# Optimization experiments

Measured on AMD Instinct MI355X. Metric: run time of the kernel, lower is better.

## Reference

```python
import jax, jax.numpy as jnp
import numpy as np

B, C, T, Q = 4, 64, 128, 128   # batch, channels (emb_dim), frames, freq bins
K = 8                          # unfold kernel size (stride 1)
H = 128                        # SRU hidden size per direction
D_IN = C * K                   # SRU input size after unfold
L = Q - K + 1                  # unfolded sequence length
EPS = 1e-5


def setup_inputs() -> dict:
    key = jax.random.key(0)
    ks = jax.random.split(key, 6)
    s = 0.02
    return {
        "features": jax.random.normal(ks[0], (B, C, T, Q), jnp.float32),
        "ln_gamma": jnp.ones((C,), jnp.float32),
        "ln_beta": jnp.zeros((C,), jnp.float32),
        # SRU per-direction weights: W maps D_IN -> [x_tilde | f_gate | r_gate | highway], each H wide
        "w_fwd": jax.random.normal(ks[1], (D_IN, 4 * H), jnp.float32) * s,
        "b_fwd": jnp.zeros((2 * H,), jnp.float32),   # [b_f | b_r]
        "w_bwd": jax.random.normal(ks[2], (D_IN, 4 * H), jnp.float32) * s,
        "b_bwd": jnp.zeros((2 * H,), jnp.float32),
        # ConvTranspose1d weight in PyTorch layout [in_ch=2H, out_ch=C, K]
        "ct_w": jax.random.normal(ks[3], (2 * H, C, K), jnp.float32) * s,
        "ct_b": jnp.zeros((C,), jnp.float32),
    }


def _sru_dir(seq, W, b, reverse):
    """One SRU direction. seq: [N, L, D_IN] -> h: [N, L, H].
    c_t = f_t*c_{t-1} + (1-f_t)*x~_t ;  h_t = r_t*tanh(c_t) + (1-r_t)*x'_t
    (x' is the highway projection since input dim != hidden dim)."""
    U = seq @ W                                   # [N, L, 4H] -- dominant GEMM
    xt, f_pre, r_pre, xp = jnp.split(U, 4, axis=-1)
    bf, br = jnp.split(b, 2)
    f = jax.nn.sigmoid(f_pre + bf)
    r = jax.nn.sigmoid(r_pre + br)
    u = (1.0 - f) * xt
    if reverse:
        f = jnp.flip(f, 1)
        u = jnp.flip(u, 1)
    def combine(x, y):  # linear recurrence c = a*c_prev + b, y is the later element
        return (x[0] * y[0], x[1] * y[0] + y[1])
    c = jax.lax.associative_scan(combine, (f, u), axis=1)[1]
    if reverse:
        c = jnp.flip(c, 1)
    return r * jnp.tanh(c) + (1.0 - r) * xp


def reference(features, ln_gamma, ln_beta, w_fwd, b_fwd, w_bwd, b_bwd, ct_w, ct_b):
    # LayerNorm([C,1,1]): normalize over channel dim per (b,t,q)
    mu = jnp.mean(features, axis=1, keepdims=True)
    var = jnp.var(features, axis=1, keepdims=True)
    x = (features - mu) * jax.lax.rsqrt(var + EPS)
    x = x * ln_gamma[None, :, None, None] + ln_beta[None, :, None, None]

    N = B * T
    x = x.transpose(0, 2, 1, 3).reshape(N, C, Q)          # [B*T, C, Q]
    # nn.Unfold((K,1), stride 1): channel-major patch layout -> [N, C*K, L]
    u = jnp.stack([x[:, :, i:i + L] for i in range(K)], axis=2).reshape(N, C * K, L)
    seq = u.transpose(0, 2, 1)                            # [N, L, C*K]

    h = jnp.concatenate(
        [_sru_dir(seq, w_fwd, b_fwd, False), _sru_dir(seq, w_bwd, b_bwd, True)],
        axis=-1,
    )                                                      # [N, L, 2H]

    # ConvTranspose1d(2H -> C, K, stride=1) == full correlation with flipped kernel
    rhs = jnp.flip(ct_w, -1).transpose(1, 0, 2)           # [C, 2H, K]
    y = jax.lax.conv_general_dilated(
        h.transpose(0, 2, 1), rhs, (1,), [(K - 1, K - 1)],
        dimension_numbers=("NCH", "OIH", "NCH"),
    ) + ct_b[None, :, None]                               # [N, C, Q]

    y = y.reshape(B, T, C, Q).transpose(0, 2, 1, 3)       # [B, C, T, Q]
    return y + features
```

## Files before the change

kernel.cpp:

```cpp
#include <hip/hip_runtime.h>
#include <math.h>

#define BB 4
#define CC 64
#define TT 128
#define QQ 128
#define KK 8
#define HH 128
#define NN 512
#define LL 121
#define LPAD 135

typedef unsigned short ushort;
typedef __attribute__((ext_vector_type(8))) short short8;
typedef __attribute__((ext_vector_type(4))) float f32x4;
typedef __attribute__((ext_vector_type(4))) float float4v;

#define GLP(p) ((const __attribute__((address_space(1))) void*)(p))
#define LDP(p) ((__attribute__((address_space(3))) void*)(p))

__device__ __forceinline__ ushort f2bf(float x) {
  unsigned u = __float_as_uint(x);
  unsigned r = (u + 0x7FFFu + ((u >> 16) & 1u)) >> 16;
  return (ushort)r;
}

__global__ __launch_bounds__(256)
void prep_all(const float* __restrict__ f, const float* __restrict__ gamma,
              const float* __restrict__ beta, const float* __restrict__ wf,
              const float* __restrict__ wb, const float* __restrict__ ctw,
              ushort* __restrict__ xT, ushort* __restrict__ Wt,
              ushort* __restrict__ Bct, ushort* __restrict__ zpage) {
  int bid = blockIdx.x, tid = threadIdx.x;
  if (bid < 256) {
    int p = bid * 256 + tid;
    int q = p & (QQ - 1);
    int t = (p >> 7) & (TT - 1);
    int b = p >> 14;
    const float* base = f + (size_t)b * CC * TT * QQ + (size_t)t * QQ + q;
    float v[64];
#pragma unroll
    for (int c = 0; c < 64; ++c) v[c] = base[(size_t)c * TT * QQ];
    float s = 0.f, s2 = 0.f;
#pragma unroll
    for (int c = 0; c < 64; ++c) { s += v[c]; s2 += v[c] * v[c]; }
    float mu = s * (1.f / CC);
    float var = s2 * (1.f / CC) - mu * mu;
    float rs = rsqrtf(var + 1e-5f);
    int n = b * TT + t;
    ushort* dst = xT + (size_t)n * (CC * QQ) + (size_t)q * CC;
#pragma unroll
    for (int v8 = 0; v8 < 8; ++v8) {
      short8 ov;
#pragma unroll
      for (int e = 0; e < 8; ++e) {
        int c = v8 * 8 + e;
        ov[e] = (short)f2bf((v[c] - mu) * rs * gamma[c] + beta[c]);
      }
      *(short8*)(dst + v8 * 8) = ov;
    }
  } else if (bid < 2816) {
    int idx = (bid - 256) * 256 + tid;
    if (idx < 524288) {
      int r = idx >> 9, d = idx & 511;
      int k = d >> 6, c = d & 63;
      int dir = r >> 9, t = r & 511;
      int h = (t >> 7) * 32 + ((t >> 6) & 1) * 16 + (t & 15);
      int quad = (t >> 4) & 3;
      const float* w = dir ? wb : wf;
      Wt[idx] = f2bf(w[(size_t)(c * 8 + k) * 512 + quad * 128 + h]);
    } else {
      int i2 = idx - 524288;
      int c = i2 >> 11, d = i2 & 2047;
      int k = d >> 8, j = d & 255;
      Bct[i2] = f2bf(ctw[(size_t)j * (CC * KK) + c * KK + k]);
    }
  } else {
    if (tid < 128) ((unsigned*)zpage)[tid] = 0u;
  }
}

__global__ __launch_bounds__(256, 2)
void gemm_mfma(const ushort* __restrict__ xT, const ushort* __restrict__ Wt,
               const float* __restrict__ b_fwd, const float* __restrict__ b_bwd,
               ushort* __restrict__ hp, int n0) {
  __shared__ __align__(16) char smem[49152];
  ushort* As = (ushort*)smem;
  ushort* Bs = (ushort*)(smem + 16384);

  int tid = threadIdx.x;
  int nl = blockIdx.y;
  int r0 = blockIdx.x * 256;
  int lane = tid & 63, w = tid >> 6;
  int lrow = lane & 15, lk = lane >> 4;
  f32x4 acc[8][4] = {};
  const ushort* xTn = xT + (size_t)(n0 + nl) * (CC * QQ);
  for (int ks = 0; ks < 8; ++ks) {
    if (ks) __syncthreads();
#pragma unroll
    for (int i = 0; i < 4; ++i) {
      int p = i * 256 + tid;
      int row = p >> 3, s = (p & 7) ^ (row & 7);
      int grow = ((row & 0x0C) << 3) | ((row & 0x70) >> 2) | (row & 3);
      const ushort* g = xTn + (size_t)(grow + ks) * CC + s * 8;
      ushort* l = &As[(size_t)(i * 256 + (tid & 192)) * 8];
      __builtin_amdgcn_global_load_lds(GLP(g), LDP(l), 16, 0, 0);
    }
#pragma unroll
    for (int i = 0; i < 8; ++i) {
      int p = i * 256 + tid;
      int row = p >> 3, s = (p & 7) ^ (row & 7);
      const ushort* g = Wt + (size_t)(r0 + row) * 512 + ks * 64 + s * 8;
      ushort* l = &Bs[(size_t)(i * 256 + (tid & 192)) * 8];
      __builtin_amdgcn_global_load_lds(GLP(g), LDP(l), 16, 0, 0);
    }
    __syncthreads();
#pragma unroll
    for (int s = 0; s < 2; ++s) {
      short8 a[8], b[4];
#pragma unroll
      for (int m = 0; m < 8; ++m) {
        int r = m * 16 + lrow;
        int slot = (s * 4 + lk) ^ (r & 7);
        a[m] = *(const short8*)&As[r * 64 + slot * 8];
      }
#pragma unroll
      for (int nn = 0; nn < 4; ++nn) {
        int j = w * 64 + nn * 16 + lrow;
        int slot = (s * 4 + lk) ^ (j & 7);
        b[nn] = *(const short8*)&Bs[j * 64 + slot * 8];
      }
#pragma unroll
      for (int m = 0; m < 8; ++m)
#pragma unroll
        for (int nn = 0; nn < 4; ++nn)
          acc[m][nn] = __builtin_amdgcn_mfma_f32_16x16x32_bf16(
              a[m], b[nn], acc[m][nn], 0, 0, 0);
    }
  }
  int dirf = r0 >> 9;
  int hgroup = ((r0 & 511) >> 7) + (w >> 1);
  int h = hgroup * 32 + (w & 1) * 16 + lrow;
  const float* bias = dirf ? b_bwd : b_fwd;
  float bf = bias[h], br = bias[128 + h];

  float F = 1.f, U = 0.f;
  if (dirf == 0) {
#pragma unroll
    for (int m = 0; m < 8; ++m)
#pragma unroll
      for (int g = 0; g < 4; ++g) {
        int l = lk * 32 + m * 4 + g;
        float xt = acc[m][0][g], fp = acc[m][1][g];
        float fg = 1.f / (1.f + __expf(-(fp + bf)));
        float u = (1.f - fg) * xt;
        if (l > 120) { fg = 1.f; u = 0.f; }
        U = fg * U + u;
        F = fg * F;
        acc[m][0][g] = F; acc[m][1][g] = U;
      }
  } else {
#pragma unroll
    for (int m = 7; m >= 0; --m)
#pragma unroll
      for (int g = 3; g >= 0; --g) {
        int l = lk * 32 + m * 4 + g;
        float xt = acc[m][0][g], fp = acc[m][1][g];
        float fg = 1.f / (1.f + __expf(-(fp + bf)));
        float u = (1.f - fg) * xt;
        if (l > 120) { fg = 1.f; u = 0.f; }
        U = fg * U + u;
        F = fg * F;
        acc[m][0][g] = F; acc[m][1][g] = U;
      }
  }
  int e = dirf ? 3 - lk : lk;
  float lpU = 0.f;
#pragma unroll
  for (int j = 0; j < 4; ++j) {
    int jl = dirf ? 3 - j : j;
    float tF = __shfl(F, (jl << 4) + lrow);
    float tU = __shfl(U, (jl << 4) + lrow);
    if (j < e) lpU = tF * lpU + tU;
  }
  float cinit = lpU;
  ushort* hpn = hp + (size_t)nl * LPAD * 256;
  int colbase = dirf * 128 + hgroup * 32 + (w & 1) * 16;
#pragma unroll
  for (int m = 0; m < 8; ++m) {
#pragma unroll
    for (int g = 0; g < 4; ++g) {
      int l = lk * 32 + m * 4 + g;
      float c = acc[m][1][g] + acc[m][0][g] * cinit;
      float rp = acc[m][2][g];
      float rg = 1.f / (1.f + __expf(-(rp + br)));
      float e2 = __expf(2.f * c);
      float th = (e2 - 1.f) / (e2 + 1.f);
      float ho = rg * th + (1.f - rg) * acc[m][3][g];
      hpn[(size_t)(l + 7) * 256 + colbase + lrow] = f2bf(ho);
    }
  }
}

__global__ __launch_bounds__(256)
void conv_mfma(const ushort* __restrict__ hp, const ushort* __restrict__ Bct,
               const ushort* __restrict__ zpage, const float* __restrict__ ctb,
               const float* __restrict__ feat, float* __restrict__ out, int n0) {
  __shared__ ushort As[2][128 * 64];
  __shared__ ushort Bs[2][64 * 64];
  int tid = threadIdx.x;
  int nl = blockIdx.x;
  int lane = tid & 63, w = tid >> 6;
  int wr0 = (w >> 1) * 64, wc0 = (w & 1) * 32;
  int lrow = lane & 15, lk = lane >> 4;
  f32x4 acc[4][2] = {};
  const ushort* hpn = hp + (size_t)nl * LPAD * 256;

#define CONV_STAGE(KS, BSEL)                                               \
  {                                                                        \
    int kk_ = (KS) >> 2, j0_ = ((KS) & 3) * 64;                            \
    _Pragma("unroll")                                                      \
    for (int i = 0; i < 4; ++i) {                                          \
      int p = i * 256 + tid;                                               \
      int row = p >> 3, s = (p & 7) ^ (row & 7);                           \
      int rr = row - kk_;                                                  \
      const ushort* g = ((unsigned)rr <= 120u)                             \
          ? hpn + (size_t)(rr + 7) * 256 + j0_ + s * 8                     \
          : zpage + s * 8;                                                 \
      ushort* l = &As[BSEL][(size_t)(i * 256 + (tid & 192)) * 8];          \
      __builtin_amdgcn_global_load_lds(GLP(g), LDP(l), 16, 0, 0);          \
    }                                                                      \
    _Pragma("unroll")                                                      \
    for (int i = 0; i < 2; ++i) {                                          \
      int p = i * 256 + tid;                                               \
      int row = p >> 3, s = (p & 7) ^ (row & 7);                           \
      const ushort* g = Bct + (size_t)row * 2048 + (KS) * 64 + s * 8;      \
      ushort* l = &Bs[BSEL][(size_t)(i * 256 + (tid & 192)) * 8];          \
      __builtin_amdgcn_global_load_lds(GLP(g), LDP(l), 16, 0, 0);          \
    }                                                                      \
  }

  CONV_STAGE(0, 0);
  __syncthreads();
  for (int ks = 0; ks < 32; ++ks) {
    int cur = ks & 1;
    if (ks < 31) CONV_STAGE(ks + 1, cur ^ 1);
#pragma unroll
    for (int s = 0; s < 2; ++s) {
      short8 a[4], b[2];
#pragma unroll
      for (int m = 0; m < 4; ++m) {
        int r = wr0 + m * 16 + lrow;
        int slot = (s * 4 + lk) ^ (r & 7);
        a[m] = *(const short8*)&As[cur][r * 64 + slot * 8];
      }
#pragma unroll
      for (int nn = 0; nn < 2; ++nn) {
        int c = wc0 + nn * 16 + lrow;
        int slot = (s * 4 + lk) ^ (c & 7);
        b[nn] = *(const short8*)&Bs[cur][c * 64 + slot * 8];
      }
#pragma unroll
      for (int m = 0; m < 4; ++m)
#pragma unroll
        for (int nn = 0; nn < 2; ++nn)
          acc[m][nn] = __builtin_amdgcn_mfma_f32_16x16x32_bf16(
              a[m], b[nn], acc[m][nn], 0, 0, 0);
    }
    __syncthreads();
  }
#undef CONV_STAGE
  int n = n0 + nl;
  int b = n >> 7, t = n & 127;
#pragma unroll
  for (int m = 0; m < 4; ++m) {
    int q0 = wr0 + m * 16 + lk * 4;
#pragma unroll
    for (int nn = 0; nn < 2; ++nn) {
      int c = wc0 + nn * 16 + lrow;
      size_t idx = (size_t)b * (CC * TT * QQ) + (size_t)c * (TT * QQ)
                 + (size_t)t * QQ + q0;
      float4v fv = *(const float4v*)&feat[idx];
      float cb = ctb[c];
      float4v ov;
#pragma unroll
      for (int g = 0; g < 4; ++g) ov[g] = acc[m][nn][g] + cb + fv[g];
      *(float4v*)&out[idx] = ov;
    }
  }
}

extern "C" void kernel_launch(void* const* d_in, const int* in_sizes, int n_in,
                              void* d_out, int out_size, void* d_ws, size_t ws_size,
                              hipStream_t stream) {
  const float* feat  = (const float*)d_in[0];
  const float* gamma = (const float*)d_in[1];
  const float* beta  = (const float*)d_in[2];
  const float* w_fwd = (const float*)d_in[3];
  const float* b_fwd = (const float*)d_in[4];
  const float* w_bwd = (const float*)d_in[5];
  const float* b_bwd = (const float*)d_in[6];
  const float* ct_w  = (const float*)d_in[7];
  const float* ct_b  = (const float*)d_in[8];
  float* out = (float*)d_out;

  char* wsb = (char*)d_ws;
  ushort* xT  = (ushort*)wsb;
  ushort* Wt  = (ushort*)(wsb + 8388608);
  ushort* Bct = (ushort*)(wsb + 9437184);
  ushort* zpg = (ushort*)(wsb + 9699328);
  size_t persist = 9699840;
  size_t per_n = 69120u;
  int NC = 4;
  for (int cand = 512; cand >= 4; cand >>= 1) {
    if (persist + (size_t)cand * per_n <= ws_size) { NC = cand; break; }
  }
  ushort* hpc = (ushort*)(wsb + persist);

  prep_all<<<dim3(2817), dim3(256), 0, stream>>>(feat, gamma, beta, w_fwd,
                                                 w_bwd, ct_w, xT, Wt, Bct, zpg);

  for (int n0 = 0; n0 < NN; n0 += NC) {
    gemm_mfma<<<dim3(4, NC), dim3(256), 0, stream>>>(xT, Wt, b_fwd, b_bwd,
                                                     hpc, n0);
    conv_mfma<<<dim3(NC), dim3(256), 0, stream>>>(hpc, Bct, zpg, ct_b, feat,
                                                  out, n0);
  }
}
```

Baseline: 140.9 us.

## Stage h rows once per half-channel in LDS and reuse across conv taps

```diff
diff --git a/kernel.cpp b/kernel.cpp
--- a/kernel.cpp
+++ b/kernel.cpp
@@ -206,8 +206,8 @@
 void conv_mfma(const ushort* __restrict__ hp, const ushort* __restrict__ Bct,
                const ushort* __restrict__ zpage, const float* __restrict__ ctb,
                const float* __restrict__ feat, float* __restrict__ out, int n0) {
-  __shared__ ushort As[2][128 * 64];
-  __shared__ ushort Bs[2][64 * 64];
+  __shared__ __align__(16) ushort Hs[144 * 128];
+  __shared__ __align__(16) ushort Bs[2][64 * 64];
   int tid = threadIdx.x;
   int nl = blockIdx.x;
   int lane = tid & 63, w = tid >> 6;
@@ -216,60 +216,64 @@
   f32x4 acc[4][2] = {};
   const ushort* hpn = hp + (size_t)nl * LPAD * 256;
 
-#define CONV_STAGE(KS, BSEL)                                               \
+#define CONV_BSTAGE(T, BSEL)                                               \
   {                                                                        \
-    int kk_ = (KS) >> 2, j0_ = ((KS) & 3) * 64;                            \
-    _Pragma("unroll")                                                      \
-    for (int i = 0; i < 4; ++i) {                                          \
-      int p = i * 256 + tid;                                               \
-      int row = p >> 3, s = (p & 7) ^ (row & 7);                           \
-      int rr = row - kk_;                                                  \
-      const ushort* g = ((unsigned)rr <= 120u)                             \
-          ? hpn + (size_t)(rr + 7) * 256 + j0_ + s * 8                     \
-          : zpage + s * 8;                                                 \
-      ushort* l = &As[BSEL][(size_t)(i * 256 + (tid & 192)) * 8];          \
-      __builtin_amdgcn_global_load_lds(GLP(g), LDP(l), 16, 0, 0);          \
-    }                                                                      \
+    int kk_ = (T) >> 1, sub_ = (T) & 1;                                    \
     _Pragma("unroll")                                                      \
     for (int i = 0; i < 2; ++i) {                                          \
       int p = i * 256 + tid;                                               \
-      int row = p >> 3, s = (p & 7) ^ (row & 7);                           \
-      const ushort* g = Bct + (size_t)row * 2048 + (KS) * 64 + s * 8;      \
+      int row = p >> 3, ds = p & 7;                                        \
+      const ushort* g = Bct + (size_t)row * 2048 + kk_ * 256 + jh * 128    \
+                      + sub_ * 64 + (ds ^ (row & 7)) * 8;                  \
       ushort* l = &Bs[BSEL][(size_t)(i * 256 + (tid & 192)) * 8];          \
       __builtin_amdgcn_global_load_lds(GLP(g), LDP(l), 16, 0, 0);          \
     }                                                                      \
   }
 
-  CONV_STAGE(0, 0);
-  __syncthreads();
-  for (int ks = 0; ks < 32; ++ks) {
-    int cur = ks & 1;
-    if (ks < 31) CONV_STAGE(ks + 1, cur ^ 1);
-#pragma unroll
-    for (int s = 0; s < 2; ++s) {
-      short8 a[4], b[2];
-#pragma unroll
-      for (int m = 0; m < 4; ++m) {
-        int r = wr0 + m * 16 + lrow;
-        int slot = (s * 4 + lk) ^ (r & 7);
-        a[m] = *(const short8*)&As[cur][r * 64 + slot * 8];
-      }
-#pragma unroll
-      for (int nn = 0; nn < 2; ++nn) {
-        int c = wc0 + nn * 16 + lrow;
-        int slot = (s * 4 + lk) ^ (c & 7);
-        b[nn] = *(const short8*)&Bs[cur][c * 64 + slot * 8];
-      }
-#pragma unroll
-      for (int m = 0; m < 4; ++m)
-#pragma unroll
-        for (int nn = 0; nn < 2; ++nn)
-          acc[m][nn] = __builtin_amdgcn_mfma_f32_16x16x32_bf16(
-              a[m], b[nn], acc[m][nn], 0, 0, 0);
-    }
+  for (int jh = 0; jh < 2; ++jh) {
+#pragma unroll
+    for (int r = 0; r < 9; ++r) {
+      int p = r * 256 + tid;
+      int row = p >> 4, ds = p & 15;
+      int cs = (ds & 8) | ((ds & 7) ^ (row & 7));
+      const ushort* g = ((unsigned)(row - 7) <= 120u)
+          ? hpn + (size_t)row * 256 + jh * 128 + cs * 8
+          : zpage;
+      ushort* l = &Hs[(size_t)(r * 256 + (tid & 192)) * 8];
+      __builtin_amdgcn_global_load_lds(GLP(g), LDP(l), 16, 0, 0);
+    }
+    CONV_BSTAGE(0, 0);
     __syncthreads();
-  }
-#undef CONV_STAGE
+    for (int t = 0; t < 16; ++t) {
+      int cur = t & 1;
+      if (t < 15) CONV_BSTAGE(t + 1, cur ^ 1);
+      int kk = t >> 1, sub = t & 1;
+#pragma unroll
+      for (int s = 0; s < 2; ++s) {
+        short8 a[4], b[2];
+#pragma unroll
+        for (int m = 0; m < 4; ++m) {
+          int row = wr0 + m * 16 + lrow + 7 - kk;
+          int slot = (sub * 8) | ((s * 4 + lk) ^ (row & 7));
+          a[m] = *(const short8*)&Hs[row * 128 + slot * 8];
+        }
+#pragma unroll
+        for (int nn = 0; nn < 2; ++nn) {
+          int c = wc0 + nn * 16 + lrow;
+          int slot = (s * 4 + lk) ^ (c & 7);
+          b[nn] = *(const short8*)&Bs[cur][c * 64 + slot * 8];
+        }
+#pragma unroll
+        for (int m = 0; m < 4; ++m)
+#pragma unroll
+          for (int nn = 0; nn < 2; ++nn)
+            acc[m][nn] = __builtin_amdgcn_mfma_f32_16x16x32_bf16(
+                a[m], b[nn], acc[m][nn], 0, 0, 0);
+      }
+      __syncthreads();
+    }
+  }
+#undef CONV_BSTAGE
   int n = n0 + nl;
   int b = n >> 7, t = n & 127;
 #pragma unroll
```

Result: faster. 123.4 us (-12.4%).
